# Performance work log

Hardware: AMD Instinct MI355X
Metric: run time of the kernel (lower is better)

## Reference

```python
import jax, jax.numpy as jnp
import numpy as np

B, T, E = 4, 2048, 1024
HS = 64            # attention_head_size
NH = E // HS       # num_heads = 16 (all heads share one weight set in the original)


def setup_inputs() -> dict:
    key = jax.random.key(0)
    ks = jax.random.split(key, 6)
    s = 0.02
    x = jax.random.normal(ks[0], (B, T, E), dtype=jnp.float32)
    Wq = jax.random.normal(ks[1], (E, HS), dtype=jnp.float32) * s
    Wk = jax.random.normal(ks[2], (E, HS), dtype=jnp.float32) * s
    Wv = jax.random.normal(ks[3], (E, HS), dtype=jnp.float32) * s
    Wp = jax.random.normal(ks[4], (E, E), dtype=jnp.float32) * s
    bp = jax.random.normal(ks[5], (E,), dtype=jnp.float32) * s
    return {"x": x, "Wq": Wq, "Wk": Wk, "Wv": Wv, "Wp": Wp, "bp": bp}


def reference(x, Wq, Wk, Wv, Wp, bp):
    # Single shared head (the torch module replicates one Head instance NH times).
    hs = Wq.shape[1]
    num_heads = Wp.shape[0] // hs
    q = jnp.einsum('bte,eh->bth', x, Wq)   # [B,T,HS]
    k = jnp.einsum('bte,eh->bth', x, Wk)
    v = jnp.einsum('bte,eh->bth', x, Wv)
    att = jnp.einsum('bqh,bkh->bqk', q, k) * (hs ** -0.5)  # [B,T,T]
    t = x.shape[1]
    causal = jnp.tril(jnp.ones((t, t), dtype=bool))
    att = jnp.where(causal, att, jnp.finfo(att.dtype).min)
    att = jax.nn.softmax(att, axis=-1)
    head = jnp.einsum('bqk,bkh->bqh', att, v)              # [B,T,HS]
    # Concat of identical head outputs == tile along feature dim.
    out = jnp.tile(head, (1, 1, num_heads))                # [B,T,E]
    out = jnp.einsum('bte,ef->btf', out, Wp) + bp          # output projection
    return out
```

## Files before the change

kernel.cpp:

```cpp
#include <hip/hip_runtime.h>
#include <hip/hip_bf16.h>

#define T_SEQ 2048
#define E_DIM 1024
#define HSZ   64
#define NBAT  4
#define QB    64
#define NQT   32

typedef __attribute__((ext_vector_type(8))) short short8;
typedef __attribute__((ext_vector_type(4))) float f32x4;

__device__ inline short f2bf(float f) {
  union { float f; unsigned u; } v; v.f = f;
  unsigned r = v.u + 0x7FFFu + ((v.u >> 16) & 1u);
  return (short)(r >> 16);
}

__global__ __launch_bounds__(256) void wpr_kernel(const float* __restrict__ Wp,
                                                  short* __restrict__ Wpb) {
  int idx = blockIdx.x * 256 + threadIdx.x;
  int f = idx & (E_DIM - 1);
  int j = idx >> 10;
  float s = 0.f;
#pragma unroll
  for (int h = 0; h < 16; ++h) s += Wp[(size_t)(h * HSZ + j) * E_DIM + f];
  Wpb[(size_t)f * HSZ + j] = f2bf(s);
}

__global__ __launch_bounds__(256) void wt_kernel(const float* __restrict__ Wq,
    const float* __restrict__ Wk, const float* __restrict__ Wv,
    short* __restrict__ Wt) {
  int idx = blockIdx.x * 256 + threadIdx.x;
  int kk = idx & 63;
  int tmp = idx >> 6;
  int kt = tmp / 192;
  int n = tmp - kt * 192;
  const float* W = (n < 64) ? Wq : (n < 128) ? Wk : Wv;
  Wt[idx] = f2bf(W[(size_t)(kt * 64 + kk) * HSZ + (n & 63)]);
}

__global__ __launch_bounds__(256) void qkv_mfma(const float* __restrict__ X,
    const short* __restrict__ Wt, short* __restrict__ Qo,
    short* __restrict__ Ko, short* __restrict__ Vt) {
  __shared__ short Xs[16 * 64];
  __shared__ short Ws[192 * 64];

  const int tid = threadIdx.x;
  const int m0 = blockIdx.x * 16;
  const int lane = tid & 63, w = tid >> 6;
  const int l15 = lane & 15, l4 = lane >> 4;

  f32x4 acc[3];
  acc[0] = (f32x4)0.f; acc[1] = (f32x4)0.f; acc[2] = (f32x4)0.f;

  for (int kt = 0; kt < 16; ++kt) {
    const int k0 = kt * 64;
    if (tid < 128) {
      int r = tid >> 3, c = tid & 7;
      const float* s = &X[(size_t)(m0 + r) * E_DIM + k0 + c * 8];
      float4 a = *(const float4*)s, d = *(const float4*)(s + 4);
      short8 f;
      f[0] = f2bf(a.x); f[1] = f2bf(a.y); f[2] = f2bf(a.z); f[3] = f2bf(a.w);
      f[4] = f2bf(d.x); f[5] = f2bf(d.y); f[6] = f2bf(d.z); f[7] = f2bf(d.w);
      *(short8*)&Xs[r * 64 + ((c ^ (r & 7)) * 8)] = f;
    }
    {
      const short* wsrc = Wt + (size_t)kt * 12288;
#pragma unroll
      for (int i = 0; i < 6; ++i) {
        int ci = tid + i * 256;
        int r = ci >> 3, c = ci & 7;
        short8 f = *(const short8*)&wsrc[ci * 8];
        *(short8*)&Ws[r * 64 + ((c ^ (r & 7)) * 8)] = f;
      }
    }
    __syncthreads();
#pragma unroll
    for (int ks = 0; ks < 2; ++ks) {
      short8 af = *(short8*)&Xs[l15 * 64 + (((ks * 4 + l4) ^ (l15 & 7)) * 8)];
#pragma unroll
      for (int i = 0; i < 3; ++i) {
        int n = (w * 3 + i) * 16 + l15;
        short8 bf = *(short8*)&Ws[n * 64 + (((ks * 4 + l4) ^ (n & 7)) * 8)];
        acc[i] = __builtin_amdgcn_mfma_f32_16x16x32_bf16(af, bf, acc[i], 0, 0, 0);
      }
    }
    __syncthreads();
  }

  const int b = m0 >> 11, t = m0 & 2047;
#pragma unroll
  for (int i = 0; i < 3; ++i) {
    const int nb = w * 3 + i;
    const int col = (nb & 3) * 16 + l15;
    const int sel = nb >> 2;
#pragma unroll
    for (int reg = 0; reg < 4; ++reg) {
      const int row = l4 * 4 + reg;
      short v = f2bf(acc[i][reg]);
      if (sel == 0)      Qo[(size_t)(m0 + row) * HSZ + col] = v;
      else if (sel == 1) Ko[(size_t)(m0 + row) * HSZ + col] = v;
      else               Vt[((size_t)b * HSZ + col) * T_SEQ + t + row] = v;
    }
  }
}

__global__ __launch_bounds__(256) void attn_part(const short* __restrict__ Q,
    const short* __restrict__ K, const short* __restrict__ Vt,
    float* __restrict__ Opart, float* __restrict__ mpart,
    float* __restrict__ lpart, int splits) {
  const int qt = blockIdx.x;
  const int sp = blockIdx.y;
  const int b  = blockIdx.z;
  const int ntile = qt + 1;
  const int t0 = (sp * ntile) / splits;
  const int t1 = ((sp + 1) * ntile) / splits;
  const int q0 = qt * QB;
  const int pidx = (b * NQT + qt) * splits + sp;
  float* Op = Opart + (size_t)pidx * QB * HSZ;
  float* mp = mpart + (size_t)pidx * QB;
  float* lp = lpart + (size_t)pidx * QB;
  const int tid = threadIdx.x;

  if (t0 >= t1) {
    if (tid < QB) { mp[tid] = -1e30f; lp[tid] = 0.f; }
    return;
  }

  const short* Qb  = Q  + (size_t)b * T_SEQ * HSZ;
  const short* Kb  = K  + (size_t)b * T_SEQ * HSZ;
  const short* Vtb = Vt + (size_t)b * HSZ * T_SEQ;

  __shared__ short Ks[64 * 64];
  __shared__ short Vs[64 * 64];
  __shared__ short Ps[4][16 * 64];

  const int lane = tid & 63;
  const int w    = tid >> 6;
  const int l15  = lane & 15;
  const int l4   = lane >> 4;

  short8 qf[2];
#pragma unroll
  for (int ks = 0; ks < 2; ++ks)
    qf[ks] = *(const short8*)&Qb[(size_t)(q0 + w * 16 + l15) * HSZ + ks * 32 + l4 * 8];

  f32x4 o[4];
  float m_[4], l_[4];
#pragma unroll
  for (int i = 0; i < 4; ++i) { o[i] = (f32x4)0.f; m_[i] = -1e30f; l_[i] = 0.f; }

  for (int kt = t0; kt < t1; ++kt) {
    const int kv0 = kt * 64;
#pragma unroll
    for (int ci = tid; ci < 512; ci += 256) {
      int r = ci >> 3, c = ci & 7;
      short8 f = *(const short8*)&Kb[(size_t)(kv0 + r) * HSZ + c * 8];
      *(short8*)&Ks[r * 64 + ((c ^ (r & 7)) * 8)] = f;
    }
#pragma unroll
    for (int ci = tid; ci < 512; ci += 256) {
      int r = ci >> 3, c = ci & 7;
      short8 f = *(const short8*)&Vtb[(size_t)r * T_SEQ + kv0 + c * 8];
      *(short8*)&Vs[r * 64 + ((c ^ (r & 7)) * 8)] = f;
    }
    __syncthreads();

    f32x4 sacc[4];
#pragma unroll
    for (int nb = 0; nb < 4; ++nb) sacc[nb] = (f32x4)0.f;
#pragma unroll
    for (int nb = 0; nb < 4; ++nb) {
      const int krow = nb * 16 + l15;
#pragma unroll
      for (int ks = 0; ks < 2; ++ks) {
        short8 kf = *(short8*)&Ks[krow * 64 + (((ks * 4 + l4) ^ (krow & 7)) * 8)];
        sacc[nb] = __builtin_amdgcn_mfma_f32_16x16x32_bf16(qf[ks], kf, sacc[nb],
                                                           0, 0, 0);
      }
    }

    const bool diag = (kt == qt);
#pragma unroll
    for (int reg = 0; reg < 4; ++reg) {
      const int grow = q0 + w * 16 + l4 * 4 + reg;
      float sv[4];
      float rmax = -1e30f;
#pragma unroll
      for (int nb = 0; nb < 4; ++nb) {
        sv[nb] = sacc[nb][reg] * 0.125f;
        if (diag && (kv0 + nb * 16 + l15 > grow)) sv[nb] = -1e30f;
        rmax = fmaxf(rmax, sv[nb]);
      }
#pragma unroll
      for (int d = 1; d < 16; d <<= 1) rmax = fmaxf(rmax, __shfl_xor(rmax, d));
      const float mn = fmaxf(m_[reg], rmax);
      const float sc = __expf(m_[reg] - mn);
      float rsum = 0.f;
#pragma unroll
      for (int nb = 0; nb < 4; ++nb) {
        sv[nb] = __expf(sv[nb] - mn);
        rsum += sv[nb];
      }
#pragma unroll
      for (int d = 1; d < 16; d <<= 1) rsum += __shfl_xor(rsum, d);
      l_[reg] = l_[reg] * sc + rsum;
      m_[reg] = mn;
#pragma unroll
      for (int hb = 0; hb < 4; ++hb) o[hb][reg] *= sc;
      const int prow = l4 * 4 + reg;
#pragma unroll
      for (int nb = 0; nb < 4; ++nb) {
        const int col = nb * 16 + l15;
        Ps[w][prow * 64 + (((col >> 3) ^ (prow & 7)) * 8) + (col & 7)] =
            f2bf(sv[nb]);
      }
    }

#pragma unroll
    for (int ks = 0; ks < 2; ++ks) {
      const int prow = l15;
      short8 pf = *(short8*)&Ps[w][prow * 64 + (((ks * 4 + l4) ^ (prow & 7)) * 8)];
#pragma unroll
      for (int hb = 0; hb < 4; ++hb) {
        const int vrow = hb * 16 + l15;
        short8 vf = *(short8*)&Vs[vrow * 64 + (((ks * 4 + l4) ^ (vrow & 7)) * 8)];
        o[hb] = __builtin_amdgcn_mfma_f32_16x16x32_bf16(pf, vf, o[hb], 0, 0, 0);
      }
    }
    __syncthreads();
  }

#pragma unroll
  for (int hb = 0; hb < 4; ++hb)
#pragma unroll
    for (int reg = 0; reg < 4; ++reg)
      Op[(size_t)(w * 16 + l4 * 4 + reg) * HSZ + hb * 16 + l15] = o[hb][reg];
  if (l15 == 0) {
#pragma unroll
    for (int reg = 0; reg < 4; ++reg) {
      mp[w * 16 + l4 * 4 + reg] = m_[reg];
      lp[w * 16 + l4 * 4 + reg] = l_[reg];
    }
  }
}

__global__ __launch_bounds__(256) void attn_combine(
    const float* __restrict__ Opart, const float* __restrict__ mpart,
    const float* __restrict__ lpart, short* __restrict__ Hd16, int splits) {
  const int qt = blockIdx.x, b = blockIdx.y;
  const int row = threadIdx.x >> 2;
  const int c0 = (threadIdx.x & 3) * 16;
  const int pbase = (b * NQT + qt) * splits;

  float M = -1e30f;
  for (int s = 0; s < splits; ++s)
    M = fmaxf(M, mpart[(size_t)(pbase + s) * QB + row]);

  float L = 0.f;
  float acc[16];
#pragma unroll
  for (int c = 0; c < 16; ++c) acc[c] = 0.f;

  for (int s = 0; s < splits; ++s) {
    const float ms = mpart[(size_t)(pbase + s) * QB + row];
    const float ls = lpart[(size_t)(pbase + s) * QB + row];
    const float w = __expf(ms - M);
    L += w * ls;
    const float* Op = Opart + ((size_t)(pbase + s) * QB + row) * HSZ + c0;
#pragma unroll
    for (int cc = 0; cc < 16; cc += 4) {
      float4 v = *(const float4*)&Op[cc];
      acc[cc + 0] += w * v.x; acc[cc + 1] += w * v.y;
      acc[cc + 2] += w * v.z; acc[cc + 3] += w * v.w;
    }
  }

  const float inv = 1.f / L;
  short* dst = Hd16 + ((size_t)b * T_SEQ + qt * QB + row) * HSZ + c0;
  short8 v0, v1;
#pragma unroll
  for (int cc = 0; cc < 8; ++cc) {
    v0[cc] = f2bf(acc[cc] * inv);
    v1[cc] = f2bf(acc[8 + cc] * inv);
  }
  *(short8*)dst = v0;
  *(short8*)(dst + 8) = v1;
}

__global__ __launch_bounds__(256) void proj_mfma(const short* __restrict__ Hd16,
    const short* __restrict__ Wpb, const float* __restrict__ bp,
    float* __restrict__ Out) {
  const int tid = threadIdx.x;
  const int lane = tid & 63, w = tid >> 6;
  const int l15 = lane & 15, l4 = lane >> 4;
  const int m0 = blockIdx.x * 64 + w * 16;
  const int n0 = blockIdx.y * 128;

  const short* asrc = &Hd16[(size_t)(m0 + l15) * HSZ + l4 * 8];
  short8 af0 = *(const short8*)asrc;
  short8 af1 = *(const short8*)(asrc + 32);

#pragma unroll
  for (int nb = 0; nb < 8; ++nb) {
    const int n = n0 + nb * 16 + l15;
    const short* bsrc = &Wpb[(size_t)n * HSZ + l4 * 8];
    short8 b0 = *(const short8*)bsrc;
    short8 b1 = *(const short8*)(bsrc + 32);
    f32x4 acc = (f32x4)0.f;
    acc = __builtin_amdgcn_mfma_f32_16x16x32_bf16(af0, b0, acc, 0, 0, 0);
    acc = __builtin_amdgcn_mfma_f32_16x16x32_bf16(af1, b1, acc, 0, 0, 0);
    const float bpv = bp[n];
#pragma unroll
    for (int reg = 0; reg < 4; ++reg)
      Out[(size_t)(m0 + l4 * 4 + reg) * E_DIM + n] = acc[reg] + bpv;
  }
}

extern "C" void kernel_launch(void* const* d_in, const int* in_sizes, int n_in,
                              void* d_out, int out_size, void* d_ws,
                              size_t ws_size, hipStream_t stream) {
  (void)in_sizes; (void)n_in; (void)out_size;
  const float* x  = (const float*)d_in[0];
  const float* Wq = (const float*)d_in[1];
  const float* Wk = (const float*)d_in[2];
  const float* Wv = (const float*)d_in[3];
  const float* Wp = (const float*)d_in[4];
  const float* bp = (const float*)d_in[5];
  float* out = (float*)d_out;

  float* ws   = (float*)d_ws;
  short* Qb16 = (short*)(ws);
  short* Kb16 = (short*)(ws + 262144);
  short* Vt16 = (short*)(ws + 524288);
  short* Hd16 = (short*)(ws + 786432);
  short* Wpb  = (short*)(ws + 1048576);
  short* Wt   = (short*)(ws + 1081344);
  const size_t base = 1179648;

  int splits = 8;
  const size_t per_split = (size_t)NBAT * NQT * (QB * HSZ + 2 * QB);
  while (splits > 1 && (base + per_split * splits) * 4 > ws_size) splits >>= 1;

  float* Opart = ws + base;
  float* mpart = Opart + (size_t)NBAT * NQT * splits * QB * HSZ;
  float* lpart = mpart + (size_t)NBAT * NQT * splits * QB;

  wpr_kernel<<<dim3(256), dim3(256), 0, stream>>>(Wp, Wpb);
  wt_kernel<<<dim3(768), dim3(256), 0, stream>>>(Wq, Wk, Wv, Wt);
  qkv_mfma<<<dim3(512), dim3(256), 0, stream>>>(x, Wt, Qb16, Kb16, Vt16);
  attn_part<<<dim3(NQT, splits, NBAT), dim3(256), 0, stream>>>(
      Qb16, Kb16, Vt16, Opart, mpart, lpart, splits);
  attn_combine<<<dim3(NQT, NBAT), dim3(256), 0, stream>>>(
      Opart, mpart, lpart, Hd16, splits);
  proj_mfma<<<dim3(128, 8), dim3(256), 0, stream>>>(Hd16, Wpb, bp, out);
}
```

Before: 150.3 us.

## Merge weight-prep kernels, double-buffer K/V tiles, fuse split combine into projection

The two weight-preparation kernels become one launch. The attention split kernel now double-buffers its K/V shared-memory tiles, prefetching the next tile into registers while computing the current one, and drops one barrier per iteration. The split-softmax combine is folded into the output projection kernel, which removes the intermediate bf16 head buffer and one launch. In exchange, each projection block recomputes the combine for its rows, four times per row across the N-blocks, and the attention kernel uses more LDS.

Result: no change. 149.8 us (-0.3%).

```diff
diff --git a/kernel.cpp b/kernel.cpp
--- a/kernel.cpp
+++ b/kernel.cpp
@@ -17,27 +17,27 @@
   return (short)(r >> 16);
 }
 
-__global__ __launch_bounds__(256) void wpr_kernel(const float* __restrict__ Wp,
-                                                  short* __restrict__ Wpb) {
-  int idx = blockIdx.x * 256 + threadIdx.x;
-  int f = idx & (E_DIM - 1);
-  int j = idx >> 10;
-  float s = 0.f;
-#pragma unroll
-  for (int h = 0; h < 16; ++h) s += Wp[(size_t)(h * HSZ + j) * E_DIM + f];
-  Wpb[(size_t)f * HSZ + j] = f2bf(s);
-}
-
-__global__ __launch_bounds__(256) void wt_kernel(const float* __restrict__ Wq,
-    const float* __restrict__ Wk, const float* __restrict__ Wv,
+__global__ __launch_bounds__(256) void prep_kernel(const float* __restrict__ Wp,
+    const float* __restrict__ Wq, const float* __restrict__ Wk,
+    const float* __restrict__ Wv, short* __restrict__ Wpb,
     short* __restrict__ Wt) {
   int idx = blockIdx.x * 256 + threadIdx.x;
-  int kk = idx & 63;
-  int tmp = idx >> 6;
-  int kt = tmp / 192;
-  int n = tmp - kt * 192;
-  const float* W = (n < 64) ? Wq : (n < 128) ? Wk : Wv;
-  Wt[idx] = f2bf(W[(size_t)(kt * 64 + kk) * HSZ + (n & 63)]);
+  if (idx < 65536) {
+    int f = idx & (E_DIM - 1);
+    int j = idx >> 10;
+    float s = 0.f;
+#pragma unroll
+    for (int h = 0; h < 16; ++h) s += Wp[(size_t)(h * HSZ + j) * E_DIM + f];
+    Wpb[(size_t)f * HSZ + j] = f2bf(s);
+  } else {
+    int id2 = idx - 65536;
+    int kk = id2 & 63;
+    int tmp = id2 >> 6;
+    int kt = tmp / 192;
+    int n = tmp - kt * 192;
+    const float* W = (n < 64) ? Wq : (n < 128) ? Wk : Wv;
+    Wt[id2] = f2bf(W[(size_t)(kt * 64 + kk) * HSZ + (n & 63)]);
+  }
 }
 
 __global__ __launch_bounds__(256) void qkv_mfma(const float* __restrict__ X,
@@ -132,8 +132,8 @@
   const short* Kb  = K  + (size_t)b * T_SEQ * HSZ;
   const short* Vtb = Vt + (size_t)b * HSZ * T_SEQ;
 
-  __shared__ short Ks[64 * 64];
-  __shared__ short Vs[64 * 64];
+  __shared__ short Ks[2][64 * 64];
+  __shared__ short Vs[2][64 * 64];
   __shared__ short Ps[4][16 * 64];
 
   const int lane = tid & 63;
@@ -141,6 +141,24 @@
   const int l15  = lane & 15;
   const int l4   = lane >> 4;
 
+  const int r0s = tid >> 3,          c0s = tid & 7;
+  const int r1s = (tid + 256) >> 3,  c1s = tid & 7;
+
+  short8 kr0, kr1, vr0, vr1;
+#define LOADT(kt_) do { \
+    const int kv0_ = (kt_) * 64; \
+    kr0 = *(const short8*)&Kb[(size_t)(kv0_ + r0s) * HSZ + c0s * 8]; \
+    kr1 = *(const short8*)&Kb[(size_t)(kv0_ + r1s) * HSZ + c1s * 8]; \
+    vr0 = *(const short8*)&Vtb[(size_t)r0s * T_SEQ + kv0_ + c0s * 8]; \
+    vr1 = *(const short8*)&Vtb[(size_t)r1s * T_SEQ + kv0_ + c1s * 8]; \
+  } while (0)
+#define WRITET(buf_) do { \
+    *(short8*)&Ks[buf_][r0s * 64 + ((c0s ^ (r0s & 7)) * 8)] = kr0; \
+    *(short8*)&Ks[buf_][r1s * 64 + ((c1s ^ (r1s & 7)) * 8)] = kr1; \
+    *(short8*)&Vs[buf_][r0s * 64 + ((c0s ^ (r0s & 7)) * 8)] = vr0; \
+    *(short8*)&Vs[buf_][r1s * 64 + ((c1s ^ (r1s & 7)) * 8)] = vr1; \
+  } while (0)
+
   short8 qf[2];
 #pragma unroll
   for (int ks = 0; ks < 2; ++ks)
@@ -151,21 +169,18 @@
 #pragma unroll
   for (int i = 0; i < 4; ++i) { o[i] = (f32x4)0.f; m_[i] = -1e30f; l_[i] = 0.f; }
 
+  LOADT(t0);
+  WRITET(0);
+  __syncthreads();
+  int cur = 0;
+
   for (int kt = t0; kt < t1; ++kt) {
     const int kv0 = kt * 64;
-#pragma unroll
-    for (int ci = tid; ci < 512; ci += 256) {
-      int r = ci >> 3, c = ci & 7;
-      short8 f = *(const short8*)&Kb[(size_t)(kv0 + r) * HSZ + c * 8];
-      *(short8*)&Ks[r * 64 + ((c ^ (r & 7)) * 8)] = f;
-    }
-#pragma unroll
-    for (int ci = tid; ci < 512; ci += 256) {
-      int r = ci >> 3, c = ci & 7;
-      short8 f = *(const short8*)&Vtb[(size_t)r * T_SEQ + kv0 + c * 8];
-      *(short8*)&Vs[r * 64 + ((c ^ (r & 7)) * 8)] = f;
-    }
-    __syncthreads();
+    const bool more = (kt + 1 < t1);
+    if (more) LOADT(kt + 1);
+
+    const short* Kc = Ks[cur];
+    const short* Vc = Vs[cur];
 
     f32x4 sacc[4];
 #pragma unroll
@@ -175,7 +190,7 @@
       const int krow = nb * 16 + l15;
 #pragma unroll
       for (int ks = 0; ks < 2; ++ks) {
-        short8 kf = *(short8*)&Ks[krow * 64 + (((ks * 4 + l4) ^ (krow & 7)) * 8)];
+        short8 kf = *(const short8*)&Kc[krow * 64 + (((ks * 4 + l4) ^ (krow & 7)) * 8)];
         sacc[nb] = __builtin_amdgcn_mfma_f32_16x16x32_bf16(qf[ks], kf, sacc[nb],
                                                            0, 0, 0);
       }
@@ -225,12 +240,19 @@
 #pragma unroll
       for (int hb = 0; hb < 4; ++hb) {
         const int vrow = hb * 16 + l15;
-        short8 vf = *(short8*)&Vs[vrow * 64 + (((ks * 4 + l4) ^ (vrow & 7)) * 8)];
+        short8 vf = *(const short8*)&Vc[vrow * 64 + (((ks * 4 + l4) ^ (vrow & 7)) * 8)];
         o[hb] = __builtin_amdgcn_mfma_f32_16x16x32_bf16(pf, vf, o[hb], 0, 0, 0);
       }
     }
-    __syncthreads();
-  }
+
+    if (more) {
+      WRITET(cur ^ 1);
+      __syncthreads();
+      cur ^= 1;
+    }
+  }
+#undef LOADT
+#undef WRITET
 
 #pragma unroll
   for (int hb = 0; hb < 4; ++hb)
@@ -246,64 +268,51 @@
   }
 }
 
-__global__ __launch_bounds__(256) void attn_combine(
+__global__ __launch_bounds__(256) void proj_fused(
     const float* __restrict__ Opart, const float* __restrict__ mpart,
-    const float* __restrict__ lpart, short* __restrict__ Hd16, int splits) {
-  const int qt = blockIdx.x, b = blockIdx.y;
-  const int row = threadIdx.x >> 2;
-  const int c0 = (threadIdx.x & 3) * 16;
-  const int pbase = (b * NQT + qt) * splits;
-
-  float M = -1e30f;
-  for (int s = 0; s < splits; ++s)
-    M = fmaxf(M, mpart[(size_t)(pbase + s) * QB + row]);
-
-  float L = 0.f;
-  float acc[16];
-#pragma unroll
-  for (int c = 0; c < 16; ++c) acc[c] = 0.f;
-
-  for (int s = 0; s < splits; ++s) {
-    const float ms = mpart[(size_t)(pbase + s) * QB + row];
-    const float ls = lpart[(size_t)(pbase + s) * QB + row];
-    const float w = __expf(ms - M);
-    L += w * ls;
-    const float* Op = Opart + ((size_t)(pbase + s) * QB + row) * HSZ + c0;
-#pragma unroll
-    for (int cc = 0; cc < 16; cc += 4) {
-      float4 v = *(const float4*)&Op[cc];
-      acc[cc + 0] += w * v.x; acc[cc + 1] += w * v.y;
-      acc[cc + 2] += w * v.z; acc[cc + 3] += w * v.w;
-    }
-  }
-
-  const float inv = 1.f / L;
-  short* dst = Hd16 + ((size_t)b * T_SEQ + qt * QB + row) * HSZ + c0;
-  short8 v0, v1;
-#pragma unroll
-  for (int cc = 0; cc < 8; ++cc) {
-    v0[cc] = f2bf(acc[cc] * inv);
-    v1[cc] = f2bf(acc[8 + cc] * inv);
-  }
-  *(short8*)dst = v0;
-  *(short8*)(dst + 8) = v1;
-}
-
-__global__ __launch_bounds__(256) void proj_mfma(const short* __restrict__ Hd16,
-    const short* __restrict__ Wpb, const float* __restrict__ bp,
-    float* __restrict__ Out) {
+    const float* __restrict__ lpart, const short* __restrict__ Wpb,
+    const float* __restrict__ bp, float* __restrict__ Out, int splits) {
+  const int bx = blockIdx.x;
+  const int n0 = blockIdx.y * 256;
   const int tid = threadIdx.x;
   const int lane = tid & 63, w = tid >> 6;
   const int l15 = lane & 15, l4 = lane >> 4;
-  const int m0 = blockIdx.x * 64 + w * 16;
-  const int n0 = blockIdx.y * 128;
-
-  const short* asrc = &Hd16[(size_t)(m0 + l15) * HSZ + l4 * 8];
-  short8 af0 = *(const short8*)asrc;
-  short8 af1 = *(const short8*)(asrc + 32);
-
-#pragma unroll
-  for (int nb = 0; nb < 8; ++nb) {
+  const int r = w * 16 + l15;
+  const int pbase = bx * splits;
+
+  float M = -1e30f;
+  for (int s = 0; s < splits; ++s)
+    M = fmaxf(M, mpart[(size_t)(pbase + s) * QB + r]);
+  float L = 0.f;
+  float a0[8], a1[8];
+#pragma unroll
+  for (int j = 0; j < 8; ++j) { a0[j] = 0.f; a1[j] = 0.f; }
+  for (int s = 0; s < splits; ++s) {
+    const float ms = mpart[(size_t)(pbase + s) * QB + r];
+    const float ls = lpart[(size_t)(pbase + s) * QB + r];
+    const float wgt = __expf(ms - M);
+    L += wgt * ls;
+    const float* Opr = Opart + ((size_t)(pbase + s) * QB + r) * HSZ;
+    float4 p0 = *(const float4*)&Opr[l4 * 8];
+    float4 p1 = *(const float4*)&Opr[l4 * 8 + 4];
+    float4 p2 = *(const float4*)&Opr[32 + l4 * 8];
+    float4 p3 = *(const float4*)&Opr[32 + l4 * 8 + 4];
+    a0[0] += wgt * p0.x; a0[1] += wgt * p0.y; a0[2] += wgt * p0.z; a0[3] += wgt * p0.w;
+    a0[4] += wgt * p1.x; a0[5] += wgt * p1.y; a0[6] += wgt * p1.z; a0[7] += wgt * p1.w;
+    a1[0] += wgt * p2.x; a1[1] += wgt * p2.y; a1[2] += wgt * p2.z; a1[3] += wgt * p2.w;
+    a1[4] += wgt * p3.x; a1[5] += wgt * p3.y; a1[6] += wgt * p3.z; a1[7] += wgt * p3.w;
+  }
+  const float inv = 1.f / L;
+  short8 af0, af1;
+#pragma unroll
+  for (int j = 0; j < 8; ++j) {
+    af0[j] = f2bf(a0[j] * inv);
+    af1[j] = f2bf(a1[j] * inv);
+  }
+
+  const int mbase = bx * 64 + w * 16 + l4 * 4;
+#pragma unroll 4
+  for (int nb = 0; nb < 16; ++nb) {
     const int n = n0 + nb * 16 + l15;
     const short* bsrc = &Wpb[(size_t)n * HSZ + l4 * 8];
     short8 b0 = *(const short8*)bsrc;
@@ -314,7 +323,7 @@
     const float bpv = bp[n];
 #pragma unroll
     for (int reg = 0; reg < 4; ++reg)
-      Out[(size_t)(m0 + l4 * 4 + reg) * E_DIM + n] = acc[reg] + bpv;
+      Out[(size_t)(mbase + reg) * E_DIM + n] = acc[reg] + bpv;
   }
 }
 
@@ -334,10 +343,9 @@
   short* Qb16 = (short*)(ws);
   short* Kb16 = (short*)(ws + 262144);
   short* Vt16 = (short*)(ws + 524288);
-  short* Hd16 = (short*)(ws + 786432);
-  short* Wpb  = (short*)(ws + 1048576);
-  short* Wt   = (short*)(ws + 1081344);
-  const size_t base = 1179648;
+  short* Wpb  = (short*)(ws + 786432);
+  short* Wt   = (short*)(ws + 819200);
+  const size_t base = 917504;
 
   int splits = 8;
   const size_t per_split = (size_t)NBAT * NQT * (QB * HSZ + 2 * QB);
@@ -347,12 +355,10 @@
   float* mpart = Opart + (size_t)NBAT * NQT * splits * QB * HSZ;
   float* lpart = mpart + (size_t)NBAT * NQT * splits * QB;
 
-  wpr_kernel<<<dim3(256), dim3(256), 0, stream>>>(Wp, Wpb);
-  wt_kernel<<<dim3(768), dim3(256), 0, stream>>>(Wq, Wk, Wv, Wt);
+  prep_kernel<<<dim3(1024), dim3(256), 0, stream>>>(Wp, Wq, Wk, Wv, Wpb, Wt);
   qkv_mfma<<<dim3(512), dim3(256), 0, stream>>>(x, Wt, Qb16, Kb16, Vt16);
   attn_part<<<dim3(NQT, splits, NBAT), dim3(256), 0, stream>>>(
       Qb16, Kb16, Vt16, Opart, mpart, lpart, splits);
-  attn_combine<<<dim3(NQT, NBAT), dim3(256), 0, stream>>>(
-      Opart, mpart, lpart, Hd16, splits);
-  proj_mfma<<<dim3(128, 8), dim3(256), 0, stream>>>(Hd16, Wpb, bp, out);
-}
+  proj_fused<<<dim3(128, 4), dim3(256), 0, stream>>>(
+      Opart, mpart, lpart, Wpb, bp, out, splits);
+}
```

## Fuse weight prep kernels, enlarge QKV tiles, double-buffer attention K/V, more splits

Applied to the files above, without the earlier changes.

Merges the two weight-preparation kernels into one launch. The QKV GEMM now computes 32 rows per block so each loaded weight tile is reused across twice as many rows. The attention kernel double-buffers K/V tiles in shared memory, prefetching the next tile into registers while the current one is computed, and launches the heaviest query tiles first. Split count rises from 8 to 16 for more parallelism, at the cost of more partial-result traffic and more combine work.

Measured after the change: 153.6 us. 1.02x slower.

```diff
diff --git a/kernel.cpp b/kernel.cpp
--- a/kernel.cpp
+++ b/kernel.cpp
@@ -17,46 +17,49 @@
   return (short)(r >> 16);
 }
 
-__global__ __launch_bounds__(256) void wpr_kernel(const float* __restrict__ Wp,
-                                                  short* __restrict__ Wpb) {
-  int idx = blockIdx.x * 256 + threadIdx.x;
-  int f = idx & (E_DIM - 1);
-  int j = idx >> 10;
-  float s = 0.f;
-#pragma unroll
-  for (int h = 0; h < 16; ++h) s += Wp[(size_t)(h * HSZ + j) * E_DIM + f];
-  Wpb[(size_t)f * HSZ + j] = f2bf(s);
-}
-
-__global__ __launch_bounds__(256) void wt_kernel(const float* __restrict__ Wq,
-    const float* __restrict__ Wk, const float* __restrict__ Wv,
+__global__ __launch_bounds__(256) void prep_kernel(const float* __restrict__ Wp,
+    const float* __restrict__ Wq, const float* __restrict__ Wk,
+    const float* __restrict__ Wv, short* __restrict__ Wpb,
     short* __restrict__ Wt) {
   int idx = blockIdx.x * 256 + threadIdx.x;
-  int kk = idx & 63;
-  int tmp = idx >> 6;
-  int kt = tmp / 192;
-  int n = tmp - kt * 192;
-  const float* W = (n < 64) ? Wq : (n < 128) ? Wk : Wv;
-  Wt[idx] = f2bf(W[(size_t)(kt * 64 + kk) * HSZ + (n & 63)]);
+  if (idx < 65536) {
+    int f = idx & (E_DIM - 1);
+    int j = idx >> 10;
+    float s = 0.f;
+#pragma unroll
+    for (int h = 0; h < 16; ++h) s += Wp[(size_t)(h * HSZ + j) * E_DIM + f];
+    Wpb[(size_t)f * HSZ + j] = f2bf(s);
+  } else {
+    int id2 = idx - 65536;
+    int kk = id2 & 63;
+    int tmp = id2 >> 6;
+    int kt = tmp / 192;
+    int n = tmp - kt * 192;
+    const float* W = (n < 64) ? Wq : (n < 128) ? Wk : Wv;
+    Wt[id2] = f2bf(W[(size_t)(kt * 64 + kk) * HSZ + (n & 63)]);
+  }
 }
 
 __global__ __launch_bounds__(256) void qkv_mfma(const float* __restrict__ X,
     const short* __restrict__ Wt, short* __restrict__ Qo,
     short* __restrict__ Ko, short* __restrict__ Vt) {
-  __shared__ short Xs[16 * 64];
+  __shared__ short Xs[32 * 64];
   __shared__ short Ws[192 * 64];
 
   const int tid = threadIdx.x;
-  const int m0 = blockIdx.x * 16;
+  const int m0 = blockIdx.x * 32;
   const int lane = tid & 63, w = tid >> 6;
   const int l15 = lane & 15, l4 = lane >> 4;
-
-  f32x4 acc[3];
-  acc[0] = (f32x4)0.f; acc[1] = (f32x4)0.f; acc[2] = (f32x4)0.f;
+  const int mh = (w & 1) * 16;
+  const int ng = (w >> 1) * 6;
+
+  f32x4 acc[6];
+#pragma unroll
+  for (int i = 0; i < 6; ++i) acc[i] = (f32x4)0.f;
 
   for (int kt = 0; kt < 16; ++kt) {
     const int k0 = kt * 64;
-    if (tid < 128) {
+    {
       int r = tid >> 3, c = tid & 7;
       const float* s = &X[(size_t)(m0 + r) * E_DIM + k0 + c * 8];
       float4 a = *(const float4*)s, d = *(const float4*)(s + 4);
@@ -78,10 +81,11 @@
     __syncthreads();
 #pragma unroll
     for (int ks = 0; ks < 2; ++ks) {
-      short8 af = *(short8*)&Xs[l15 * 64 + (((ks * 4 + l4) ^ (l15 & 7)) * 8)];
-#pragma unroll
-      for (int i = 0; i < 3; ++i) {
-        int n = (w * 3 + i) * 16 + l15;
+      const int ar = mh + l15;
+      short8 af = *(short8*)&Xs[ar * 64 + (((ks * 4 + l4) ^ (ar & 7)) * 8)];
+#pragma unroll
+      for (int i = 0; i < 6; ++i) {
+        int n = (ng + i) * 16 + l15;
         short8 bf = *(short8*)&Ws[n * 64 + (((ks * 4 + l4) ^ (n & 7)) * 8)];
         acc[i] = __builtin_amdgcn_mfma_f32_16x16x32_bf16(af, bf, acc[i], 0, 0, 0);
       }
@@ -91,13 +95,13 @@
 
   const int b = m0 >> 11, t = m0 & 2047;
 #pragma unroll
-  for (int i = 0; i < 3; ++i) {
-    const int nb = w * 3 + i;
+  for (int i = 0; i < 6; ++i) {
+    const int nb = ng + i;
     const int col = (nb & 3) * 16 + l15;
     const int sel = nb >> 2;
 #pragma unroll
     for (int reg = 0; reg < 4; ++reg) {
-      const int row = l4 * 4 + reg;
+      const int row = mh + l4 * 4 + reg;
       short v = f2bf(acc[i][reg]);
       if (sel == 0)      Qo[(size_t)(m0 + row) * HSZ + col] = v;
       else if (sel == 1) Ko[(size_t)(m0 + row) * HSZ + col] = v;
@@ -110,7 +114,7 @@
     const short* __restrict__ K, const short* __restrict__ Vt,
     float* __restrict__ Opart, float* __restrict__ mpart,
     float* __restrict__ lpart, int splits) {
-  const int qt = blockIdx.x;
+  const int qt = NQT - 1 - blockIdx.x;
   const int sp = blockIdx.y;
   const int b  = blockIdx.z;
   const int ntile = qt + 1;
@@ -132,8 +136,8 @@
   const short* Kb  = K  + (size_t)b * T_SEQ * HSZ;
   const short* Vtb = Vt + (size_t)b * HSZ * T_SEQ;
 
-  __shared__ short Ks[64 * 64];
-  __shared__ short Vs[64 * 64];
+  __shared__ short Ks[2][64 * 64];
+  __shared__ short Vs[2][64 * 64];
   __shared__ short Ps[4][16 * 64];
 
   const int lane = tid & 63;
@@ -141,6 +145,24 @@
   const int l15  = lane & 15;
   const int l4   = lane >> 4;
 
+  const int r0s = tid >> 3,          c0s = tid & 7;
+  const int r1s = (tid + 256) >> 3,  c1s = tid & 7;
+
+  short8 kr0, kr1, vr0, vr1;
+#define LOADT(kt_) do { \
+    const int kv0_ = (kt_) * 64; \
+    kr0 = *(const short8*)&Kb[(size_t)(kv0_ + r0s) * HSZ + c0s * 8]; \
+    kr1 = *(const short8*)&Kb[(size_t)(kv0_ + r1s) * HSZ + c1s * 8]; \
+    vr0 = *(const short8*)&Vtb[(size_t)r0s * T_SEQ + kv0_ + c0s * 8]; \
+    vr1 = *(const short8*)&Vtb[(size_t)r1s * T_SEQ + kv0_ + c1s * 8]; \
+  } while (0)
+#define WRITET(buf_) do { \
+    *(short8*)&Ks[buf_][r0s * 64 + ((c0s ^ (r0s & 7)) * 8)] = kr0; \
+    *(short8*)&Ks[buf_][r1s * 64 + ((c1s ^ (r1s & 7)) * 8)] = kr1; \
+    *(short8*)&Vs[buf_][r0s * 64 + ((c0s ^ (r0s & 7)) * 8)] = vr0; \
+    *(short8*)&Vs[buf_][r1s * 64 + ((c1s ^ (r1s & 7)) * 8)] = vr1; \
+  } while (0)
+
   short8 qf[2];
 #pragma unroll
   for (int ks = 0; ks < 2; ++ks)
@@ -151,21 +173,18 @@
 #pragma unroll
   for (int i = 0; i < 4; ++i) { o[i] = (f32x4)0.f; m_[i] = -1e30f; l_[i] = 0.f; }
 
+  LOADT(t0);
+  WRITET(0);
+  __syncthreads();
+  int cur = 0;
+
   for (int kt = t0; kt < t1; ++kt) {
     const int kv0 = kt * 64;
-#pragma unroll
-    for (int ci = tid; ci < 512; ci += 256) {
-      int r = ci >> 3, c = ci & 7;
-      short8 f = *(const short8*)&Kb[(size_t)(kv0 + r) * HSZ + c * 8];
-      *(short8*)&Ks[r * 64 + ((c ^ (r & 7)) * 8)] = f;
-    }
-#pragma unroll
-    for (int ci = tid; ci < 512; ci += 256) {
-      int r = ci >> 3, c = ci & 7;
-      short8 f = *(const short8*)&Vtb[(size_t)r * T_SEQ + kv0 + c * 8];
-      *(short8*)&Vs[r * 64 + ((c ^ (r & 7)) * 8)] = f;
-    }
-    __syncthreads();
+    const bool more = (kt + 1 < t1);
+    if (more) LOADT(kt + 1);
+
+    const short* Kc = Ks[cur];
+    const short* Vc = Vs[cur];
 
     f32x4 sacc[4];
 #pragma unroll
@@ -175,7 +194,7 @@
       const int krow = nb * 16 + l15;
 #pragma unroll
       for (int ks = 0; ks < 2; ++ks) {
-        short8 kf = *(short8*)&Ks[krow * 64 + (((ks * 4 + l4) ^ (krow & 7)) * 8)];
+        short8 kf = *(const short8*)&Kc[krow * 64 + (((ks * 4 + l4) ^ (krow & 7)) * 8)];
         sacc[nb] = __builtin_amdgcn_mfma_f32_16x16x32_bf16(qf[ks], kf, sacc[nb],
                                                            0, 0, 0);
       }
@@ -225,12 +244,19 @@
 #pragma unroll
       for (int hb = 0; hb < 4; ++hb) {
         const int vrow = hb * 16 + l15;
-        short8 vf = *(short8*)&Vs[vrow * 64 + (((ks * 4 + l4) ^ (vrow & 7)) * 8)];
+        short8 vf = *(const short8*)&Vc[vrow * 64 + (((ks * 4 + l4) ^ (vrow & 7)) * 8)];
         o[hb] = __builtin_amdgcn_mfma_f32_16x16x32_bf16(pf, vf, o[hb], 0, 0, 0);
       }
     }
-    __syncthreads();
-  }
+
+    if (more) {
+      WRITET(cur ^ 1);
+      __syncthreads();
+      cur ^= 1;
+    }
+  }
+#undef LOADT
+#undef WRITET
 
 #pragma unroll
   for (int hb = 0; hb < 4; ++hb)
@@ -339,7 +365,7 @@
   short* Wt   = (short*)(ws + 1081344);
   const size_t base = 1179648;
 
-  int splits = 8;
+  int splits = 16;
   const size_t per_split = (size_t)NBAT * NQT * (QB * HSZ + 2 * QB);
   while (splits > 1 && (base + per_split * splits) * 4 > ws_size) splits >>= 1;
 
@@ -347,9 +373,8 @@
   float* mpart = Opart + (size_t)NBAT * NQT * splits * QB * HSZ;
   float* lpart = mpart + (size_t)NBAT * NQT * splits * QB;
 
-  wpr_kernel<<<dim3(256), dim3(256), 0, stream>>>(Wp, Wpb);
-  wt_kernel<<<dim3(768), dim3(256), 0, stream>>>(Wq, Wk, Wv, Wt);
-  qkv_mfma<<<dim3(512), dim3(256), 0, stream>>>(x, Wt, Qb16, Kb16, Vt16);
+  prep_kernel<<<dim3(1024), dim3(256), 0, stream>>>(Wp, Wq, Wk, Wv, Wpb, Wt);
+  qkv_mfma<<<dim3(256), dim3(256), 0, stream>>>(x, Wt, Qb16, Kb16, Vt16);
   attn_part<<<dim3(NQT, splits, NBAT), dim3(256), 0, stream>>>(
       Qb16, Kb16, Vt16, Opart, mpart, lpart, splits);
   attn_combine<<<dim3(NQT, NBAT), dim3(256), 0, stream>>>(
```
